# Kernel tuning notes

Measured on AMD Instinct MI355X. Metric: run time of the kernel, lower is better.

The kernel has to match this reference:

```python
import jax, jax.numpy as jnp
import numpy as np

DIM = 1024          # hidden_size
HEADS = 16
KDIM = DIM // 2     # expand_k = 0.5
VDIM = DIM          # expand_v = 1.0
DK = KDIM // HEADS  # 32 head key dim
DV = VDIM // HEADS  # 64 head value dim
LOW = 16            # gate_low_rank_dim
NORMALIZER = 16.0   # gate_logit_normalizer
EPS = 1e-5
B, T = 2, 4096


def setup_inputs() -> dict:
    key = jax.random.key(0)
    ks = jax.random.split(key, 9)
    def lin(k, sh, fan_in):
        return jax.random.normal(k, sh, jnp.float32) * (fan_in ** -0.5)
    return {
        "x":    jax.random.normal(ks[0], (B, T, DIM), jnp.float32),
        "Wq":   lin(ks[1], (DIM, KDIM), DIM),
        "Wk":   lin(ks[2], (DIM, KDIM), DIM),
        "Wv":   lin(ks[3], (DIM, VDIM), DIM),
        "Wgk1": lin(ks[4], (DIM, LOW), DIM),   # low-rank gate proj (no bias)
        "Wgk2": lin(ks[5], (LOW, KDIM), LOW),  # low-rank gate proj (with bias)
        "bgk2": jnp.zeros((KDIM,), jnp.float32),
        "Wg":   lin(ks[6], (DIM, VDIM), DIM),  # output gate proj (no bias)
        "gnw":  jnp.ones((DV,), jnp.float32),  # per-head RMSNorm weight
        "Wo":   lin(ks[7], (VDIM, DIM), VDIM),
    }


def _gla_scan(q, k, v, gk):
    # q,k,gk: (B,T,H,DK)  v: (B,T,H,DV)
    # recurrent form of chunked GLA: h_t = exp(gk_t) (x) h_{t-1} + k_t (outer) v_t
    scale = DK ** -0.5
    def step(h, inp):
        qt, kt, vt, gt = inp                      # (B,H,DK)/(B,H,DV)
        h = h * jnp.exp(gt)[..., None] + kt[..., None] * vt[..., None, :]
        ot = jnp.einsum('bhk,bhkv->bhv', qt * scale, h)
        return h, ot
    h0 = jnp.zeros((q.shape[0], HEADS, DK, DV), q.dtype)
    xs = tuple(jnp.moveaxis(a, 1, 0) for a in (q, k, v, gk))  # time-major
    _, o = jax.lax.scan(step, h0, xs)
    return jnp.moveaxis(o, 0, 1)                  # (B,T,H,DV)


def reference(x, Wq, Wk, Wv, Wgk1, Wgk2, bgk2, Wg, gnw, Wo):
    Bx, Tx, _ = x.shape
    q = (x @ Wq).reshape(Bx, Tx, HEADS, DK)
    k = (x @ Wk).reshape(Bx, Tx, HEADS, DK)
    v = (x @ Wv).reshape(Bx, Tx, HEADS, DV)
    # data-dependent log-decay gate: logsigmoid(low-rank proj) / normalizer
    gk = jax.nn.log_sigmoid((x @ Wgk1) @ Wgk2 + bgk2)
    gk = gk.reshape(Bx, Tx, HEADS, DK) / NORMALIZER
    o = _gla_scan(q, k, v, gk)                    # (B,T,H,DV)
    # fused per-head RMSNorm + swish output gate
    g = (x @ Wg).reshape(Bx, Tx, HEADS, DV)
    o = o * jax.lax.rsqrt(jnp.mean(o * o, axis=-1, keepdims=True) + EPS) * gnw
    o = o * (g * jax.nn.sigmoid(g))
    return o.reshape(Bx, Tx, VDIM) @ Wo
```

## Files before the change

### kernel.cpp

```cpp
#include <hip/hip_runtime.h>

typedef unsigned short u16;
typedef unsigned int u32;
typedef __attribute__((ext_vector_type(8))) short short8;
typedef __attribute__((ext_vector_type(4))) float f32x4;

#define KD 512
#define HEADS 16
#define DK 32
#define DV 64
#define TT 4096
#define MROWS 8192
#define CHUNK 64
#define NCH 64
#define NBH 32
#define QSTR 3200
#define SCALE 0.17677669529663687f

__device__ __forceinline__ u16 f2bf(float f) {
    union { float f; unsigned int u; } x; x.f = f;
    unsigned int u = x.u;
    unsigned int r = (u + 0x7fffu + ((u >> 16) & 1u)) >> 16;
    return (u16)r;
}
__device__ __forceinline__ float bf2f(u16 s) {
    union { unsigned int u; float f; } x; x.u = ((unsigned int)s) << 16;
    return x.f;
}
__device__ __forceinline__ void gload16(const u16* g, u16* l) {
    __builtin_amdgcn_global_load_lds((const __attribute__((address_space(1))) u32*)g,
                                     (__attribute__((address_space(3))) u32*)l, 16, 0, 0);
}

__global__ __launch_bounds__(256) void f32_to_bf16_vec(const float* __restrict__ src,
                                                       u16* __restrict__ dst, int n4) {
    int i = blockIdx.x * 256 + threadIdx.x;
    if (i < n4) {
        const float4 v = ((const float4*)src)[i];
        ushort4 o;
        o.x = f2bf(v.x); o.y = f2bf(v.y); o.z = f2bf(v.z); o.w = f2bf(v.w);
        ((ushort4*)dst)[i] = o;
    }
}

__global__ __launch_bounds__(256) void weight_prep(const float* __restrict__ Wq,
                                                   const float* __restrict__ Wk,
                                                   const float* __restrict__ Wv,
                                                   const float* __restrict__ Wg,
                                                   const float* __restrict__ W1,
                                                   const float* __restrict__ Wo,
                                                   u16* __restrict__ dst) {
    __shared__ float tile[32][33];
    int n0 = blockIdx.x * 32, k0 = blockIdx.y * 32;
    int tx = threadIdx.x & 31, ty = threadIdx.x >> 5;
    int n = n0 + tx;
    const float* src; int sN, cc;
    if (n < 512)       { src = Wq; sN = 512;  cc = n; }
    else if (n < 1024) { src = Wk; sN = 512;  cc = n - 512; }
    else if (n < 2048) { src = Wv; sN = 1024; cc = n - 1024; }
    else if (n < 3072) { src = Wg; sN = 1024; cc = n - 2048; }
    else if (n < 3088) { src = W1; sN = 16;   cc = n - 3072; }
    else if (n < 3200) { src = nullptr; sN = 0; cc = 0; }
    else               { src = Wo; sN = 1024; cc = n - 3200; }
    for (int r = ty; r < 32; r += 8)
        tile[r][tx] = src ? src[(size_t)(k0 + r) * sN + cc] : 0.f;
    __syncthreads();
    for (int r = ty; r < 32; r += 8)
        dst[(size_t)(n0 + r) * 1024 + k0 + tx] = f2bf(tile[tx][r]);
}

template<int OUTBF>
__global__ __launch_bounds__(256) void gemm_sb(const u16* __restrict__ A,
                                               const u16* __restrict__ Bt,
                                               void* __restrict__ C,
                                               int M, int N, int K, int nbx) {
    __shared__ u16 As[128 * 64];
    __shared__ u16 Bs[128 * 64];
    int nwg = gridDim.x;
    int bid = blockIdx.x;
    int cpx = nwg >> 3;
    int wg = (bid & 7) * cpx + (bid >> 3);
    int bx = wg % nbx, by = wg / nbx;
    int tid = threadIdx.x;
    int wave = tid >> 6, lane = tid & 63;
    int wr = wave >> 1, wc = wave & 1;
    int brow = by * 128, bcol = bx * 128;
    int srow = tid >> 3;
    int sgrp = (tid & 7) ^ (srow & 7);
    const u16* aS = A + (size_t)(brow + srow) * K + sgrp * 8;
    const u16* bS = Bt + (size_t)(bcol + srow) * K + sgrp * 8;
    f32x4 acc[4][4];
    #pragma unroll
    for (int mi = 0; mi < 4; ++mi)
        #pragma unroll
        for (int ni = 0; ni < 4; ++ni)
            acc[mi][ni] = (f32x4){0.f, 0.f, 0.f, 0.f};
    int l15 = lane & 15, hi = lane >> 4;
    int rxor = l15 & 7;
    for (int kt = 0; kt < K; kt += 64) {
        __syncthreads();
        #pragma unroll
        for (int i_ = 0; i_ < 4; ++i_) {
            gload16(aS + (size_t)i_ * 32 * K + kt, As + tid * 8 + i_ * 2048);
            gload16(bS + (size_t)i_ * 32 * K + kt, Bs + tid * 8 + i_ * 2048);
        }
        __syncthreads();
        #pragma unroll
        for (int ks = 0; ks < 2; ++ks) {
            short8 af[4], bfr[4];
            int g = ks * 4 + hi;
            #pragma unroll
            for (int i = 0; i < 4; ++i)
                af[i] = *(const short8*)(As + (size_t)(wr * 64 + i * 16 + l15) * 64 + ((g ^ rxor) << 3));
            #pragma unroll
            for (int i = 0; i < 4; ++i)
                bfr[i] = *(const short8*)(Bs + (size_t)(wc * 64 + i * 16 + l15) * 64 + ((g ^ rxor) << 3));
            #pragma unroll
            for (int mi = 0; mi < 4; ++mi)
                #pragma unroll
                for (int ni = 0; ni < 4; ++ni)
                    acc[mi][ni] = __builtin_amdgcn_mfma_f32_16x16x32_bf16(af[mi], bfr[ni], acc[mi][ni], 0, 0, 0);
        }
    }
    int r0 = brow + wr * 64 + (hi << 2);
    int c0 = bcol + wc * 64 + l15;
    #pragma unroll
    for (int mi = 0; mi < 4; ++mi)
        #pragma unroll
        for (int ni = 0; ni < 4; ++ni)
            #pragma unroll
            for (int rr = 0; rr < 4; ++rr) {
                size_t idx = (size_t)(r0 + mi * 16 + rr) * N + (c0 + ni * 16);
                float val = acc[mi][ni][rr];
                if (OUTBF) ((u16*)C)[idx] = f2bf(val);
                else       ((float*)C)[idx] = val;
            }
}

__device__ __forceinline__ void gate_z8(const u16* __restrict__ xg,
                                        const float* __restrict__ W2,
                                        const float* __restrict__ b2,
                                        int cc, float* out8) {
    short8 x0 = *(const short8*)xg;
    short8 x1 = *(const short8*)(xg + 8);
    float z[8];
    float4 z0 = *(const float4*)(b2 + cc);
    float4 z1 = *(const float4*)(b2 + cc + 4);
    z[0]=z0.x; z[1]=z0.y; z[2]=z0.z; z[3]=z0.w;
    z[4]=z1.x; z[5]=z1.y; z[6]=z1.z; z[7]=z1.w;
    #pragma unroll
    for (int u = 0; u < 16; ++u) {
        float xu = bf2f((u16)(u < 8 ? x0[u] : x1[u - 8]));
        const float4 w0 = *(const float4*)(W2 + (size_t)u * 512 + cc);
        const float4 w1 = *(const float4*)(W2 + (size_t)u * 512 + cc + 4);
        z[0] += xu * w0.x; z[1] += xu * w0.y; z[2] += xu * w0.z; z[3] += xu * w0.w;
        z[4] += xu * w1.x; z[5] += xu * w1.y; z[6] += xu * w1.z; z[7] += xu * w1.w;
    }
    #pragma unroll
    for (int j = 0; j < 8; ++j) {
        float zz = z[j];
        out8[j] = (fminf(zz, 0.f) - log1pf(expf(-fabsf(zz)))) * 0.0625f;
    }
}

__global__ __launch_bounds__(256) void phaseA(const u16* __restrict__ qkvg,
                                              const float* __restrict__ W2,
                                              const float* __restrict__ b2,
                                              float* __restrict__ MT_ws,
                                              float* __restrict__ D_ws) {
    int bh = blockIdx.x >> 6, c = blockIdx.x & 63;
    int b = bh >> 4, h = bh & 15;
    int t0 = b * TT + c * CHUNK;
    __shared__ float gkS[64][36];
    __shared__ u16 kdT_bf[32 * 72];
    __shared__ u16 VT_bf[64 * 72];
    __shared__ float Z[32];
    int tid = threadIdx.x;
    int s = tid >> 2, i0 = (tid & 3) << 3;
    {
        float ls[8];
        gate_z8(qkvg + (size_t)(t0 + s) * QSTR + 3072, W2, b2, h * DK + i0, ls);
        #pragma unroll
        for (int jj = 0; jj < 8; ++jj) gkS[s][i0 + jj] = ls[jj];
    }
    short8 kv = *(const short8*)(qkvg + (size_t)(t0 + s) * QSTR + 512 + h * DK + i0);
    {
        int j0 = (tid & 3) << 4;
        short8 v0 = *(const short8*)(qkvg + (size_t)(t0 + s) * QSTR + 1024 + h * DV + j0);
        short8 v1 = *(const short8*)(qkvg + (size_t)(t0 + s) * QSTR + 1024 + h * DV + j0 + 8);
        #pragma unroll
        for (int jj = 0; jj < 8; ++jj) {
            VT_bf[(j0 + jj) * 72 + s] = (u16)v0[jj];
            VT_bf[(j0 + 8 + jj) * 72 + s] = (u16)v1[jj];
        }
    }
    __syncthreads();
    if (tid < 32) {
        float run = 0.f;
        for (int t = 0; t < 64; ++t) { run += gkS[t][tid]; gkS[t][tid] = run; }
        Z[tid] = run;
    }
    __syncthreads();
    #pragma unroll
    for (int jj = 0; jj < 8; ++jj)
        kdT_bf[(i0 + jj) * 72 + s] = f2bf(expf(Z[i0 + jj] - gkS[s][i0 + jj]) * bf2f((u16)kv[jj]));
    __syncthreads();
    int wave = tid >> 6, lane = tid & 63, l15 = lane & 15, hi = lane >> 4;
    int it = wave & 1, jp = wave >> 1;
    size_t base = ((size_t)(bh * NCH + c)) * 2048;
    #pragma unroll
    for (int jj2 = 0; jj2 < 2; ++jj2) {
        int jt = jp * 2 + jj2;
        f32x4 mc = (f32x4){0.f, 0.f, 0.f, 0.f};
        #pragma unroll
        for (int kc = 0; kc < 2; ++kc) {
            short8 ak = *(const short8*)&kdT_bf[(it * 16 + l15) * 72 + kc * 32 + hi * 8];
            short8 bv = *(const short8*)&VT_bf[(jt * 16 + l15) * 72 + kc * 32 + hi * 8];
            mc = __builtin_amdgcn_mfma_f32_16x16x32_bf16(ak, bv, mc, 0, 0, 0);
        }
        #pragma unroll
        for (int rr = 0; rr < 4; ++rr)
            MT_ws[base + (size_t)(jt * 16 + l15) * 32 + it * 16 + hi * 4 + rr] = mc[rr];
    }
    if (tid < 32) D_ws[(size_t)(bh * NCH + c) * 32 + tid] = expf(Z[tid]);
}

__global__ __launch_bounds__(256) void phaseB(const float* __restrict__ MT_ws,
                                              const float* __restrict__ D_ws,
                                              float* __restrict__ HT_ws) {
    int idx = blockIdx.x * 256 + threadIdx.x;
    int bh = idx >> 11;
    int ji = idx & 2047;
    int i = ji & 31;
    float h = 0.f;
    size_t base = (size_t)bh * NCH * 2048 + ji;
    const float* dp = D_ws + (size_t)bh * NCH * 32 + i;
    for (int c = 0; c < NCH; ++c) {
        HT_ws[base + (size_t)c * 2048] = h;
        h = h * dp[c * 32] + MT_ws[base + (size_t)c * 2048];
    }
}

__global__ __launch_bounds__(256) void phaseC(const u16* __restrict__ qkvg,
                                              const float* __restrict__ W2,
                                              const float* __restrict__ b2,
                                              const float* __restrict__ HT_ws,
                                              const float* __restrict__ gnw,
                                              u16* __restrict__ o_n) {
    int bh = blockIdx.x >> 6, c = blockIdx.x & 63;
    int b = bh >> 4, h = bh & 15;
    int t0 = b * TT + c * CHUNK;
    __shared__ float gkS[64][36];
    __shared__ u16 qh_bf[64 * 40];
    __shared__ u16 kt_bf[64 * 40];
    __shared__ u16 VT_bf[64 * 72];
    __shared__ u16 Ht_bf[64 * 40];
    u16* P_bf = (u16*)&gkS[0][0];
    int tid = threadIdx.x;
    int s = tid >> 2, i0 = (tid & 3) << 3;
    {
        float ls[8];
        gate_z8(qkvg + (size_t)(t0 + s) * QSTR + 3072, W2, b2, h * DK + i0, ls);
        #pragma unroll
        for (int jj = 0; jj < 8; ++jj) gkS[s][i0 + jj] = ls[jj];
    }
    short8 qv = *(const short8*)(qkvg + (size_t)(t0 + s) * QSTR + h * DK + i0);
    short8 kv = *(const short8*)(qkvg + (size_t)(t0 + s) * QSTR + 512 + h * DK + i0);
    {
        int j0 = (tid & 3) << 4;
        short8 v0 = *(const short8*)(qkvg + (size_t)(t0 + s) * QSTR + 1024 + h * DV + j0);
        short8 v1 = *(const short8*)(qkvg + (size_t)(t0 + s) * QSTR + 1024 + h * DV + j0 + 8);
        #pragma unroll
        for (int jj = 0; jj < 8; ++jj) {
            VT_bf[(j0 + jj) * 72 + s] = (u16)v0[jj];
            VT_bf[(j0 + 8 + jj) * 72 + s] = (u16)v1[jj];
        }
    }
    {
        const float* hp = HT_ws + ((size_t)(bh * NCH + c)) * 2048 + tid * 8;
        float4 h0 = *(const float4*)hp;
        float4 h1 = *(const float4*)(hp + 4);
        int j = tid >> 2, ii0 = (tid & 3) << 3;
        ushort4 o0, o1;
        o0.x = f2bf(h0.x); o0.y = f2bf(h0.y); o0.z = f2bf(h0.z); o0.w = f2bf(h0.w);
        o1.x = f2bf(h1.x); o1.y = f2bf(h1.y); o1.z = f2bf(h1.z); o1.w = f2bf(h1.w);
        *(ushort4*)&Ht_bf[j * 40 + ii0] = o0;
        *(ushort4*)&Ht_bf[j * 40 + ii0 + 4] = o1;
    }
    __syncthreads();
    if (tid < 32) {
        float run = 0.f;
        for (int t = 0; t < 64; ++t) { run += gkS[t][tid]; gkS[t][tid] = run; }
    }
    __syncthreads();
    #pragma unroll
    for (int jj = 0; jj < 8; ++jj) {
        float Sv = gkS[s][i0 + jj];
        qh_bf[s * 40 + i0 + jj] = f2bf(bf2f((u16)qv[jj]) * expf(Sv) * SCALE);
        kt_bf[s * 40 + i0 + jj] = f2bf(bf2f((u16)kv[jj]) * expf(fminf(-Sv, 80.f)));
    }
    __syncthreads();
    int wave = tid >> 6, lane = tid & 63, l15 = lane & 15, hi = lane >> 4;
    int w = wave;
    short8 aq = *(const short8*)&qh_bf[(w * 16 + l15) * 40 + hi * 8];
    #pragma unroll
    for (int sn = 0; sn < 4; ++sn) {
        f32x4 sc = (f32x4){0.f, 0.f, 0.f, 0.f};
        if (sn <= w) {
            short8 bk = *(const short8*)&kt_bf[(sn * 16 + l15) * 40 + hi * 8];
            sc = __builtin_amdgcn_mfma_f32_16x16x32_bf16(aq, bk, sc, 0, 0, 0);
        }
        #pragma unroll
        for (int rr = 0; rr < 4; ++rr) {
            float val = sc[rr];
            if (sn > w || (sn == w && l15 > hi * 4 + rr)) val = 0.f;
            P_bf[(w * 16 + hi * 4 + rr) * 72 + sn * 16 + l15] = f2bf(val);
        }
    }
    __syncthreads();
    f32x4 acc[4];
    #pragma unroll
    for (int jn = 0; jn < 4; ++jn) {
        f32x4 a = (f32x4){0.f, 0.f, 0.f, 0.f};
        short8 bhf = *(const short8*)&Ht_bf[(jn * 16 + l15) * 40 + hi * 8];
        acc[jn] = __builtin_amdgcn_mfma_f32_16x16x32_bf16(aq, bhf, a, 0, 0, 0);
    }
    int nkc = (w < 2) ? 1 : 2;
    for (int kc = 0; kc < nkc; ++kc) {
        short8 ap = *(const short8*)&P_bf[(w * 16 + l15) * 72 + kc * 32 + hi * 8];
        #pragma unroll
        for (int jn = 0; jn < 4; ++jn) {
            short8 bv = *(const short8*)&VT_bf[(jn * 16 + l15) * 72 + kc * 32 + hi * 8];
            acc[jn] = __builtin_amdgcn_mfma_f32_16x16x32_bf16(ap, bv, acc[jn], 0, 0, 0);
        }
    }
    #pragma unroll
    for (int rr = 0; rr < 4; ++rr) {
        float sum2 = 0.f;
        #pragma unroll
        for (int jn = 0; jn < 4; ++jn) sum2 += acc[jn][rr] * acc[jn][rr];
        sum2 += __shfl_xor(sum2, 1);
        sum2 += __shfl_xor(sum2, 2);
        sum2 += __shfl_xor(sum2, 4);
        sum2 += __shfl_xor(sum2, 8);
        float rms = rsqrtf(sum2 * (1.f / 64.f) + 1e-5f);
        int t = w * 16 + hi * 4 + rr;
        #pragma unroll
        for (int jn = 0; jn < 4; ++jn) {
            int j = jn * 16 + l15;
            float g = bf2f(qkvg[(size_t)(t0 + t) * QSTR + 2048 + h * DV + j]);
            float sw = g / (1.f + expf(-g));
            float o = acc[jn][rr] * rms * gnw[j] * sw;
            o_n[(size_t)(t0 + t) * 1024 + h * DV + j] = f2bf(o);
        }
    }
}

extern "C" void kernel_launch(void* const* d_in, const int* in_sizes, int n_in,
                              void* d_out, int out_size, void* d_ws, size_t ws_size,
                              hipStream_t stream) {
    const float* x    = (const float*)d_in[0];
    const float* Wq   = (const float*)d_in[1];
    const float* Wk   = (const float*)d_in[2];
    const float* Wv   = (const float*)d_in[3];
    const float* Wgk1 = (const float*)d_in[4];
    const float* Wgk2 = (const float*)d_in[5];
    const float* bgk2 = (const float*)d_in[6];
    const float* Wg   = (const float*)d_in[7];
    const float* gnw  = (const float*)d_in[8];
    const float* Wo   = (const float*)d_in[9];

    char* ws = (char*)d_ws;
    size_t off = 0;
    u16* xb      = (u16*)(ws + off); off += (size_t)MROWS * 1024 * 2;
    u16* Wall    = (u16*)(ws + off); off += (size_t)4224 * 1024 * 2;
    u16* qkvg    = (u16*)(ws + off); off += (size_t)MROWS * QSTR * 2;
    float* MT_ws = (float*)(ws + off); off += (size_t)NBH * NCH * 2048 * 4;
    float* D_ws  = (float*)(ws + off); off += (size_t)NBH * NCH * 32 * 4;
    float* HT_ws = (float*)(ws + off); off += (size_t)NBH * NCH * 2048 * 4;
    u16* o_n     = (u16*)(ws + off); off += (size_t)MROWS * 1024 * 2;
    u16* WcatT   = Wall;
    u16* WoT     = Wall + (size_t)3200 * 1024;

    f32_to_bf16_vec<<<MROWS, 256, 0, stream>>>(x, xb, MROWS * 1024 / 4);
    weight_prep<<<dim3(132, 32), 256, 0, stream>>>(Wq, Wk, Wv, Wg, Wgk1, Wo, Wall);
    gemm_sb<1><<<25 * 64, 256, 0, stream>>>(xb, WcatT, qkvg, MROWS, QSTR, 1024, 25);
    phaseA<<<NBH * NCH, 256, 0, stream>>>(qkvg, Wgk2, bgk2, MT_ws, D_ws);
    phaseB<<<256, 256, 0, stream>>>(MT_ws, D_ws, HT_ws);
    phaseC<<<NBH * NCH, 256, 0, stream>>>(qkvg, Wgk2, bgk2, HT_ws, gnw, o_n);
    gemm_sb<0><<<8 * 64, 256, 0, stream>>>(o_n, WoT, d_out, MROWS, 1024, 1024, 8);
}
```

Baseline: 181.2 us.

## Replace GEMM with 256x256 double-buffered 8-wave pipelined MFMA kernel

```diff
diff --git a/kernel.cpp b/kernel.cpp
--- a/kernel.cpp
+++ b/kernel.cpp
@@ -14,7 +14,7 @@
 #define CHUNK 64
 #define NCH 64
 #define NBH 32
-#define QSTR 3200
+#define QSTR 3328
 #define SCALE 0.17677669529663687f
 
 __device__ __forceinline__ u16 f2bf(float f) {
@@ -60,8 +60,8 @@
     else if (n < 2048) { src = Wv; sN = 1024; cc = n - 1024; }
     else if (n < 3072) { src = Wg; sN = 1024; cc = n - 2048; }
     else if (n < 3088) { src = W1; sN = 16;   cc = n - 3072; }
-    else if (n < 3200) { src = nullptr; sN = 0; cc = 0; }
-    else               { src = Wo; sN = 1024; cc = n - 3200; }
+    else if (n < 3328) { src = nullptr; sN = 0; cc = 0; }
+    else               { src = Wo; sN = 1024; cc = n - 3328; }
     for (int r = ty; r < 32; r += 8)
         tile[r][tx] = src ? src[(size_t)(k0 + r) * sN + cc] : 0.f;
     __syncthreads();
@@ -69,63 +69,125 @@
         dst[(size_t)(n0 + r) * 1024 + k0 + tx] = f2bf(tile[tx][r]);
 }
 
+#define BARM() do { asm volatile("" ::: "memory"); __builtin_amdgcn_s_barrier(); asm volatile("" ::: "memory"); } while (0)
+#define VMW(n) asm volatile("s_waitcnt vmcnt(" #n ")" ::: "memory")
+
 template<int OUTBF>
-__global__ __launch_bounds__(256) void gemm_sb(const u16* __restrict__ A,
-                                               const u16* __restrict__ Bt,
-                                               void* __restrict__ C,
-                                               int M, int N, int K, int nbx) {
-    __shared__ u16 As[128 * 64];
-    __shared__ u16 Bs[128 * 64];
-    int nwg = gridDim.x;
-    int bid = blockIdx.x;
-    int cpx = nwg >> 3;
+__global__ __launch_bounds__(512, 2) void gemm8(const u16* __restrict__ A,
+                                                const u16* __restrict__ Bt,
+                                                void* __restrict__ C,
+                                                int M, int N, int K, int nbx) {
+    __shared__ u16 SA[2][16384];
+    __shared__ u16 SB[2][16384];
+    int nwg = gridDim.x, bid = blockIdx.x, cpx = nwg >> 3;
     int wg = (bid & 7) * cpx + (bid >> 3);
     int bx = wg % nbx, by = wg / nbx;
+    int brow = by << 8, bcol = bx << 8;
     int tid = threadIdx.x;
-    int wave = tid >> 6, lane = tid & 63;
-    int wr = wave >> 1, wc = wave & 1;
-    int brow = by * 128, bcol = bx * 128;
-    int srow = tid >> 3;
-    int sgrp = (tid & 7) ^ (srow & 7);
-    const u16* aS = A + (size_t)(brow + srow) * K + sgrp * 8;
-    const u16* bS = Bt + (size_t)(bcol + srow) * K + sgrp * 8;
-    f32x4 acc[4][4];
-    #pragma unroll
-    for (int mi = 0; mi < 4; ++mi)
+    int wv = tid >> 6, lane = tid & 63;
+    int wm = wv >> 2, wn = wv & 3;
+    int l15 = lane & 15, hi = lane >> 4;
+    int rxor = l15 & 7;
+
+    int srw = tid >> 3;
+    int sg8 = ((tid & 7) ^ (srw & 7)) << 3;
+    const u16* aBase = A + (size_t)(brow + srw) * K + sg8;
+    const u16* bBase = Bt + (size_t)(bcol + ((tid >> 8) << 6) + (srw & 31)) * K + sg8;
+
+#define STAGE_A(b, h, tt) do { \
+        const u16* s_ = aBase + (size_t)(tt) * 64 + (size_t)(h) * 64 * K; \
+        gload16(s_,                    &SA[b][(h) * 8192 + tid * 8]); \
+        gload16(s_ + (size_t)128 * K,  &SA[b][(h) * 8192 + 4096 + tid * 8]); \
+    } while (0)
+#define STAGE_B(b, h, tt) do { \
+        const u16* s_ = bBase + (size_t)(tt) * 64 + (size_t)(h) * 32 * K; \
+        gload16(s_,                    &SB[b][(h) * 8192 + tid * 8]); \
+        gload16(s_ + (size_t)128 * K,  &SB[b][(h) * 8192 + 4096 + tid * 8]); \
+    } while (0)
+
+    int aRow = (wm * 64 + l15) * 64;
+    int bRow = (wn * 32 + l15) * 64;
+    int cg0 = (hi ^ rxor) << 3;
+    int cg1 = ((4 + hi) ^ rxor) << 3;
+
+#define READ_A(dst, mh, b) do { \
+        _Pragma("unroll") \
+        for (int mil_ = 0; mil_ < 4; ++mil_) { \
+            dst[mil_ * 2 + 0] = *(const short8*)&SA[b][(mh) * 8192 + mil_ * 1024 + aRow + cg0]; \
+            dst[mil_ * 2 + 1] = *(const short8*)&SA[b][(mh) * 8192 + mil_ * 1024 + aRow + cg1]; \
+        } } while (0)
+#define READ_B(dst, nh, b) do { \
+        _Pragma("unroll") \
+        for (int nil_ = 0; nil_ < 2; ++nil_) { \
+            dst[nil_ * 2 + 0] = *(const short8*)&SB[b][(nh) * 8192 + nil_ * 1024 + bRow + cg0]; \
+            dst[nil_ * 2 + 1] = *(const short8*)&SB[b][(nh) * 8192 + nil_ * 1024 + bRow + cg1]; \
+        } } while (0)
+
+    f32x4 acc[8][4];
+    #pragma unroll
+    for (int mi = 0; mi < 8; ++mi)
         #pragma unroll
         for (int ni = 0; ni < 4; ++ni)
             acc[mi][ni] = (f32x4){0.f, 0.f, 0.f, 0.f};
-    int l15 = lane & 15, hi = lane >> 4;
-    int rxor = l15 & 7;
-    for (int kt = 0; kt < K; kt += 64) {
-        __syncthreads();
-        #pragma unroll
-        for (int i_ = 0; i_ < 4; ++i_) {
-            gload16(aS + (size_t)i_ * 32 * K + kt, As + tid * 8 + i_ * 2048);
-            gload16(bS + (size_t)i_ * 32 * K + kt, Bs + tid * 8 + i_ * 2048);
-        }
-        __syncthreads();
-        #pragma unroll
-        for (int ks = 0; ks < 2; ++ks) {
-            short8 af[4], bfr[4];
-            int g = ks * 4 + hi;
-            #pragma unroll
-            for (int i = 0; i < 4; ++i)
-                af[i] = *(const short8*)(As + (size_t)(wr * 64 + i * 16 + l15) * 64 + ((g ^ rxor) << 3));
-            #pragma unroll
-            for (int i = 0; i < 4; ++i)
-                bfr[i] = *(const short8*)(Bs + (size_t)(wc * 64 + i * 16 + l15) * 64 + ((g ^ rxor) << 3));
-            #pragma unroll
-            for (int mi = 0; mi < 4; ++mi)
-                #pragma unroll
-                for (int ni = 0; ni < 4; ++ni)
-                    acc[mi][ni] = __builtin_amdgcn_mfma_f32_16x16x32_bf16(af[mi], bfr[ni], acc[mi][ni], 0, 0, 0);
-        }
-    }
-    int r0 = brow + wr * 64 + (hi << 2);
-    int c0 = bcol + wc * 64 + l15;
-    #pragma unroll
-    for (int mi = 0; mi < 4; ++mi)
+
+#define MM(mb, nb, AF, BF) do { \
+        __builtin_amdgcn_s_setprio(1); \
+        _Pragma("unroll") \
+        for (int ks_ = 0; ks_ < 2; ++ks_) \
+        _Pragma("unroll") \
+        for (int mil_ = 0; mil_ < 4; ++mil_) \
+        _Pragma("unroll") \
+        for (int nil_ = 0; nil_ < 2; ++nil_) \
+            acc[(mb) + mil_][(nb) + nil_] = __builtin_amdgcn_mfma_f32_16x16x32_bf16( \
+                AF[mil_ * 2 + ks_], BF[nil_ * 2 + ks_], acc[(mb) + mil_][(nb) + nil_], 0, 0, 0); \
+        __builtin_amdgcn_s_setprio(0); \
+    } while (0)
+
+    int NK = K >> 6, NI = NK >> 1;
+    STAGE_B(0, 0, 0); STAGE_A(0, 0, 0); STAGE_A(0, 1, 0); STAGE_B(0, 1, 0);
+    STAGE_B(1, 0, 1); STAGE_A(1, 0, 1); STAGE_A(1, 1, 1);
+    VMW(6);
+    BARM();
+
+    short8 alo[8], ahi[8], bb[4];
+    for (int i = 0; i < NI; ++i) {
+        int ta = 2 * i + 1; if (ta >= NK) ta = NK - 1;
+        int tb = 2 * i + 2; if (tb >= NK) tb = NK - 1;
+        int tc = 2 * i + 3; if (tc >= NK) tc = NK - 1;
+        STAGE_B(1, 1, ta);
+        READ_A(alo, 0, 0); READ_B(bb, 0, 0);
+        BARM(); MM(0, 0, alo, bb); BARM();
+        STAGE_B(0, 0, tb);
+        READ_A(ahi, 1, 0);
+        BARM(); MM(4, 0, ahi, bb); BARM();
+        STAGE_A(0, 0, tb);
+        READ_B(bb, 1, 0);
+        BARM(); MM(4, 2, ahi, bb); BARM();
+        STAGE_A(0, 1, tb);
+        BARM(); MM(0, 2, alo, bb);
+        VMW(8);
+        BARM();
+        STAGE_B(0, 1, tb);
+        READ_A(alo, 0, 1); READ_B(bb, 0, 1);
+        BARM(); MM(0, 0, alo, bb); BARM();
+        STAGE_B(1, 0, tc);
+        READ_A(ahi, 1, 1);
+        BARM(); MM(4, 0, ahi, bb);
+        VMW(10);
+        BARM();
+        STAGE_A(1, 0, tc);
+        READ_B(bb, 1, 1);
+        BARM(); MM(4, 2, ahi, bb); BARM();
+        STAGE_A(1, 1, tc);
+        BARM(); MM(0, 2, alo, bb);
+        VMW(6);
+        BARM();
+    }
+
+    int r0 = brow + wm * 128 + (hi << 2);
+    int c0 = bcol + wn * 64 + l15;
+    #pragma unroll
+    for (int mi = 0; mi < 8; ++mi)
         #pragma unroll
         for (int ni = 0; ni < 4; ++ni)
             #pragma unroll
@@ -135,6 +197,11 @@
                 if (OUTBF) ((u16*)C)[idx] = f2bf(val);
                 else       ((float*)C)[idx] = val;
             }
+#undef STAGE_A
+#undef STAGE_B
+#undef READ_A
+#undef READ_B
+#undef MM
 }
 
 __device__ __forceinline__ void gate_z8(const u16* __restrict__ xg,
@@ -373,20 +440,20 @@
     char* ws = (char*)d_ws;
     size_t off = 0;
     u16* xb      = (u16*)(ws + off); off += (size_t)MROWS * 1024 * 2;
-    u16* Wall    = (u16*)(ws + off); off += (size_t)4224 * 1024 * 2;
+    u16* Wall    = (u16*)(ws + off); off += (size_t)4352 * 1024 * 2;
     u16* qkvg    = (u16*)(ws + off); off += (size_t)MROWS * QSTR * 2;
     float* MT_ws = (float*)(ws + off); off += (size_t)NBH * NCH * 2048 * 4;
     float* D_ws  = (float*)(ws + off); off += (size_t)NBH * NCH * 32 * 4;
     float* HT_ws = (float*)(ws + off); off += (size_t)NBH * NCH * 2048 * 4;
     u16* o_n     = (u16*)(ws + off); off += (size_t)MROWS * 1024 * 2;
     u16* WcatT   = Wall;
-    u16* WoT     = Wall + (size_t)3200 * 1024;
+    u16* WoT     = Wall + (size_t)3328 * 1024;
 
     f32_to_bf16_vec<<<MROWS, 256, 0, stream>>>(x, xb, MROWS * 1024 / 4);
-    weight_prep<<<dim3(132, 32), 256, 0, stream>>>(Wq, Wk, Wv, Wg, Wgk1, Wo, Wall);
-    gemm_sb<1><<<25 * 64, 256, 0, stream>>>(xb, WcatT, qkvg, MROWS, QSTR, 1024, 25);
+    weight_prep<<<dim3(136, 32), 256, 0, stream>>>(Wq, Wk, Wv, Wg, Wgk1, Wo, Wall);
+    gemm8<1><<<416, 512, 0, stream>>>(xb, WcatT, qkvg, MROWS, QSTR, 1024, 13);
     phaseA<<<NBH * NCH, 256, 0, stream>>>(qkvg, Wgk2, bgk2, MT_ws, D_ws);
     phaseB<<<256, 256, 0, stream>>>(MT_ws, D_ws, HT_ws);
     phaseC<<<NBH * NCH, 256, 0, stream>>>(qkvg, Wgk2, bgk2, HT_ws, gnw, o_n);
-    gemm_sb<0><<<8 * 64, 256, 0, stream>>>(o_n, WoT, d_out, MROWS, 1024, 1024, 8);
-}
+    gemm8<0><<<128, 512, 0, stream>>>(o_n, WoT, d_out, MROWS, 1024, 1024, 4);
+}
```

After: 181.0 us. About the same (-0.1%).
